# Kernel optimization log

Measured on AMD Instinct MI355X. Metric: run time of the kernel, lower is better.

Reference implementation:

```python
import jax, jax.numpy as jnp
import numpy as np

ALPHA = 0.2      # LeakyReLU negative slope
NEG_INF = -9e15  # mask value from the original code

def setup_inputs() -> dict:
    key = jax.random.key(0)
    k1, k2, k3, k4 = jax.random.split(key, 4)
    B, M, F_IN, F_OUT = 16, 2048, 128, 64
    h = jax.random.normal(k1, (B, M, F_IN), dtype=jnp.float32)
    adj = jax.random.randint(k2, (B, M, M), 0, 2, dtype=jnp.int32)
    W = jax.random.normal(k3, (F_IN, F_OUT), dtype=jnp.float32) * 0.1
    a = jax.random.normal(k4, (2 * F_OUT, 1), dtype=jnp.float32) * 0.1
    return {"h": h, "adj": adj, "W": W, "a": a}

def reference(h, adj, W, a):
    # h: [B,M,Fin], adj: [B,M,M], W: [Fin,E], a: [2E,1]
    Wh = jnp.matmul(h, W)                      # [B,M,E]
    E = Wh.shape[-1]
    a1, a2 = a[:E, 0], a[E:, 0]
    # decompose a^T [Wh_i || Wh_j] = (Wh_i . a1) + (Wh_j . a2)
    f1 = Wh @ a1                               # [B,M] (source/query term)
    f2 = Wh @ a2                               # [B,M] (target/key term)
    e = jax.nn.leaky_relu(f1[:, :, None] + f2[:, None, :], negative_slope=ALPHA)  # [B,M,M]
    scores = jnp.where(adj > 0, e, NEG_INF)
    attn = jax.nn.softmax(scores, axis=-1)     # [B,M,M]  (dropout p=0 / eval mode)
    h_prime = jnp.matmul(attn, Wh)             # [B,M,E]
    return jax.nn.elu(h_prime)                 # concat=True branch
```

## Files before the change

kernel.cpp:

```cpp
#include <hip/hip_runtime.h>


#define M_     2048
#define FIN_   128
#define F_     64
#define ALPHA_ 0.2f
#define HS_    132
#define WT_    132

typedef float  float4_ __attribute__((ext_vector_type(4)));
typedef short  short8  __attribute__((ext_vector_type(8)));
typedef int    int4_   __attribute__((ext_vector_type(4)));
typedef unsigned int u32x4 __attribute__((ext_vector_type(4)));
typedef unsigned short u16;
typedef unsigned int   u32;

static __device__ __forceinline__ u32 cvtpk(float lo, float hi) {
    u32 r;
    asm("v_cvt_pk_bf16_f32 %0, %1, %2" : "=v"(r) : "v"(lo), "v"(hi));
    return r;
}

static __device__ __forceinline__ int4_ ntload4(const int* p) {
    return __builtin_nontemporal_load((const int4_*)p);
}

__global__ __launch_bounds__(256, 4) void k_prep(
    const float* __restrict__ h, const float* __restrict__ W,
    const float* __restrict__ a, u16* __restrict__ hbf,
    float* __restrict__ f1all, float* __restrict__ f2all)
{
    __shared__ float a_s[2 * F_];
    __shared__ float wa1[FIN_], wa2[FIN_];
    __shared__ float hs[32 * HS_];

    const int tid = threadIdx.x;
    const u32 bid = blockIdx.x;
    const u32 lg  = (bid & 7) * 128 + (bid >> 3);
    const int b   = lg >> 6;
    const int t   = lg & 63;

    if (tid < 128) a_s[tid] = a[tid];

    const int tok = tid >> 3, f0 = (tid & 7) * 16;
    const float* hp = h + ((size_t)(b * M_ + t * 32 + tok)) * FIN_ + f0;
    float4_ x0 = *(const float4_*)hp;
    float4_ x1 = *(const float4_*)(hp + 4);
    float4_ x2 = *(const float4_*)(hp + 8);
    float4_ x3 = *(const float4_*)(hp + 12);
    __syncthreads();

    if (tid < FIN_) {
        float s1 = 0.f, s2 = 0.f;
#pragma unroll 8
        for (int n = 0; n < F_; ++n) {
            float wv = W[tid * F_ + n];
            s1 += wv * a_s[n];
            s2 += wv * a_s[F_ + n];
        }
        wa1[tid] = s1;
        wa2[tid] = s2;
    }

    float* hr = hs + tok * HS_ + f0;
    *(float4_*)(hr)      = x0;
    *(float4_*)(hr + 4)  = x1;
    *(float4_*)(hr + 8)  = x2;
    *(float4_*)(hr + 12) = x3;
    __syncthreads();

    {
        const int l = tid & 63, lc = l & 15, q = l >> 4;
        const int nt0 = (tid >> 6) * 2;
        u32x4* ob = (u32x4*)hbf + ((size_t)(b * 64 + t)) * 8 * 64;
#pragma unroll
        for (int ni = 0; ni < 2; ++ni) {
            const int nt = nt0 + ni;
            const float* cp = hs + (q * 8) * HS_ + nt * 16 + lc;
            u32x4 wv;
            wv[0] = cvtpk(cp[0 * HS_], cp[1 * HS_]);
            wv[1] = cvtpk(cp[2 * HS_], cp[3 * HS_]);
            wv[2] = cvtpk(cp[4 * HS_], cp[5 * HS_]);
            wv[3] = cvtpk(cp[6 * HS_], cp[7 * HS_]);
            ob[nt * 64 + l] = wv;
        }
    }

    {
        const int r = tid >> 3, k0 = (tid & 7) * 16;
        const float* rp = hs + r * HS_ + k0;
        float s1 = 0.f, s2 = 0.f;
#pragma unroll
        for (int k = 0; k < 16; ++k) {
            s1 += rp[k] * wa1[k0 + k];
            s2 += rp[k] * wa2[k0 + k];
        }
        s1 += __shfl_xor(s1, 1, 64); s2 += __shfl_xor(s2, 1, 64);
        s1 += __shfl_xor(s1, 2, 64); s2 += __shfl_xor(s2, 2, 64);
        s1 += __shfl_xor(s1, 4, 64); s2 += __shfl_xor(s2, 4, 64);
        if ((tid & 7) == 0) {
            f1all[b * M_ + t * 32 + r] = s1;
            f2all[b * M_ + t * 32 + r] = s2;
        }
    }
}

__global__ __launch_bounds__(256, 4) void k_main(
    const int* __restrict__ adj, const u16* __restrict__ hbf,
    const float* __restrict__ f1all, const float* __restrict__ f2all,
    const float* __restrict__ W, float* __restrict__ out)
{
    __shared__ char  dyn[WT_ * 32 * 4];
    __shared__ float dens2[64];

    float* f2s  = (float*)dyn;
    float* Tsum = (float*)dyn;

    const int tid  = threadIdx.x;
    const int w    = tid >> 6;
    const int l    = tid & 63;
    const int lc   = l & 15;
    const int quad = l >> 4;
    const int wr   = w & 1;
    const int wh   = w >> 1;

    const u32 bid = blockIdx.x;
    const u32 lg  = (bid & 7) * 128 + (bid >> 3);
    const int b   = lg >> 6;
    const int i0  = (lg & 63) * 32;
    const int rowbase = i0 + wr * 16;

    {
        const int o = tid * 8;
        float4_ v0 = *(const float4_*)(f2all + b * M_ + o);
        float4_ v1 = *(const float4_*)(f2all + b * M_ + o + 4);
        *(float4_*)(f2s + o)     = v0;
        *(float4_*)(f2s + o + 4) = v1;
    }

    const float f1r = f1all[b * M_ + rowbase + lc];
    const int* aprow = adj + ((size_t)(b * M_ + rowbase + lc)) * M_ + quad * 8;
    const u32x4* hb  = (const u32x4*)hbf + ((size_t)b * 64) * 8 * 64 + l;

    const int t0 = wh * 32;
    const int tE = t0 + 31;

    int4_ aA0 = ntload4(aprow + t0 * 32);
    int4_ aA1 = ntload4(aprow + t0 * 32 + 4);
    int4_ aB0 = ntload4(aprow + (t0 + 1) * 32);
    int4_ aB1 = ntload4(aprow + (t0 + 1) * 32 + 4);

    __syncthreads();

    float denacc = 0.f;
    float4_ acc[8];
#pragma unroll
    for (int nt = 0; nt < 8; ++nt) acc[nt] = (float4_){0.f, 0.f, 0.f, 0.f};

#define SC(GE, GO, AE, AO, IDX)                                 \
        {                                                       \
            float xe = f1r + (GE); xe = fmaxf(xe, ALPHA_ * xe); \
            float xo = f1r + (GO); xo = fmaxf(xo, ALPHA_ * xo); \
            float ee = ((AE) > 0) ? __expf(xe) : 0.f;           \
            float eo = ((AO) > 0) ? __expf(xo) : 0.f;           \
            u32 pk = cvtpk(ee, eo);                             \
            d += __uint_as_float(pk << 16);                     \
            d += __uint_as_float(pk & 0xFFFF0000u);             \
            pw[IDX] = pk;                                       \
        }

#define STAGE(T, A0, A1)                                                      \
    {                                                                         \
        const int tp = ((T) + 2 <= tE) ? (T) + 2 : tE;                        \
        u32x4 bb[8];                                                          \
        _Pragma("unroll")                                                     \
        for (int nt = 0; nt < 8; ++nt) bb[nt] = hb[((T) * 8 + nt) * 64];      \
        __builtin_amdgcn_sched_barrier(0);                                    \
        float4_ g0 = *(const float4_*)(f2s + (T) * 32 + quad * 8);            \
        float4_ g1 = *(const float4_*)(f2s + (T) * 32 + quad * 8 + 4);        \
        u32x4 pw;                                                             \
        float d = 0.f;                                                        \
        SC(g0[0], g0[1], A0[0], A0[1], 0)                                     \
        SC(g0[2], g0[3], A0[2], A0[3], 1)                                     \
        SC(g1[0], g1[1], A1[0], A1[1], 2)                                     \
        SC(g1[2], g1[3], A1[2], A1[3], 3)                                     \
        denacc += d;                                                          \
        const short8 af = __builtin_bit_cast(short8, pw);                     \
        A0 = ntload4(aprow + tp * 32);                                        \
        A1 = ntload4(aprow + tp * 32 + 4);                                    \
        __builtin_amdgcn_sched_barrier(0);                                    \
        _Pragma("unroll")                                                     \
        for (int nt = 0; nt < 8; ++nt)                                        \
            acc[nt] = __builtin_amdgcn_mfma_f32_16x16x32_bf16(                \
                af, __builtin_bit_cast(short8, bb[nt]), acc[nt], 0, 0, 0);    \
    }

    for (int o = 0; o < 16; ++o) {
        STAGE(t0 + 2 * o,     aA0, aA1)
        STAGE(t0 + 2 * o + 1, aB0, aB1)
    }
#undef STAGE
#undef SC

    denacc += __shfl_xor(denacc, 16, 64);
    denacc += __shfl_xor(denacc, 32, 64);
    if (quad == 0) dens2[wh * 32 + wr * 16 + lc] = denacc;
    __syncthreads();

    if (wh == 0) {
#pragma unroll
        for (int nt = 0; nt < 8; ++nt)
#pragma unroll
            for (int mm = 0; mm < 4; ++mm)
                Tsum[(wr * 16 + quad * 4 + mm) * WT_ + nt * 16 + lc] = acc[nt][mm];
    }
    __syncthreads();
    if (wh == 1) {
#pragma unroll
        for (int nt = 0; nt < 8; ++nt)
#pragma unroll
            for (int mm = 0; mm < 4; ++mm)
                Tsum[(wr * 16 + quad * 4 + mm) * WT_ + nt * 16 + lc] += acc[nt][mm];
    }
    __syncthreads();

    {
        const int r  = tid >> 3;
        const int n0 = (tid & 7) * 8;
        const float den  = dens2[r] + dens2[32 + r];
        const float rden = (den > 0.f) ? (1.f / den) : 0.f;
        float u[8];
#pragma unroll
        for (int nn = 0; nn < 8; ++nn) u[nn] = 0.f;
#pragma unroll 4
        for (int k = 0; k < FIN_; ++k) {
            const float tv = Tsum[r * WT_ + k];
            float4_ wv0 = *(const float4_*)(W + k * F_ + n0);
            float4_ wv1 = *(const float4_*)(W + k * F_ + n0 + 4);
            u[0] += tv * wv0[0]; u[1] += tv * wv0[1];
            u[2] += tv * wv0[2]; u[3] += tv * wv0[3];
            u[4] += tv * wv1[0]; u[5] += tv * wv1[1];
            u[6] += tv * wv1[2]; u[7] += tv * wv1[3];
        }
        float4_ o0, o1;
#pragma unroll
        for (int nn = 0; nn < 8; ++nn) {
            float hp = u[nn] * rden;
            float o  = hp > 0.f ? hp : expm1f(hp);
            if (nn < 4) o0[nn] = o; else o1[nn - 4] = o;
        }
        float* op = out + ((size_t)(b * M_ + i0 + r)) * F_ + n0;
        *(float4_*)op       = o0;
        *(float4_*)(op + 4) = o1;
    }
}

extern "C" void kernel_launch(void* const* d_in, const int* in_sizes, int n_in,
                              void* d_out, int out_size, void* d_ws, size_t ws_size,
                              hipStream_t stream)
{
    (void)out_size; (void)ws_size;
    const float* h  = (const float*)d_in[0];
    const int* adjp = (const int*)d_in[1];
    const float* Wp = (const float*)d_in[2];
    const float* ap = (const float*)d_in[3];
    for (int i = 0; i < n_in; ++i) {
        long s = in_sizes[i];
        if      (s == 4194304L)  h    = (const float*)d_in[i];
        else if (s == 67108864L) adjp = (const int*)d_in[i];
        else if (s == 8192L)     Wp   = (const float*)d_in[i];
        else if (s == 128L)      ap   = (const float*)d_in[i];
    }
    u16*   hbf   = (u16*)d_ws;
    float* f1all = (float*)((char*)d_ws + (8u << 20));
    float* f2all = f1all + 16 * M_;
    k_prep<<<1024, 256, 0, stream>>>(h, Wp, ap, hbf, f1all, f2all);
    k_main<<<1024, 256, 0, stream>>>(adjp, hbf, f1all, f2all, Wp, (float*)d_out);
}
```

Before: 435.6 us.

## Stage Wh tiles in double-buffered LDS and give each block 64 rows

Each block now handles 64 query rows, with four waves each owning 16 rows across all 64 key tiles, replacing the split-K over two wave halves. The bf16 Wh tile for each step is loaded once into a double-buffered LDS ring and shared by all four waves instead of every wave reading it from global memory. This removes the cross-wave partial-sum reduction and cuts global Wh traffic, at the cost of a block-wide barrier per tile, more LDS, lower occupancy (launch bounds 2) and half as many blocks.

```diff
diff --git a/kernel.cpp b/kernel.cpp
--- a/kernel.cpp
+++ b/kernel.cpp
@@ -105,15 +105,16 @@
     }
 }
 
-__global__ __launch_bounds__(256, 4) void k_main(
+__global__ __launch_bounds__(256, 2) void k_main(
     const int* __restrict__ adj, const u16* __restrict__ hbf,
     const float* __restrict__ f1all, const float* __restrict__ f2all,
     const float* __restrict__ W, float* __restrict__ out)
 {
-    __shared__ char  dyn[WT_ * 32 * 4];
-    __shared__ float dens2[64];
-
-    float* f2s  = (float*)dyn;
+    __shared__ char  dyn[64 * WT_ * 4];
+    __shared__ float dens[64];
+
+    u32x4* lbuf = (u32x4*)dyn;
+    float* f2s  = (float*)(dyn + 16384);
     float* Tsum = (float*)dyn;
 
     const int tid  = threadIdx.x;
@@ -121,14 +122,11 @@
     const int l    = tid & 63;
     const int lc   = l & 15;
     const int quad = l >> 4;
-    const int wr   = w & 1;
-    const int wh   = w >> 1;
 
     const u32 bid = blockIdx.x;
-    const u32 lg  = (bid & 7) * 128 + (bid >> 3);
-    const int b   = lg >> 6;
-    const int i0  = (lg & 63) * 32;
-    const int rowbase = i0 + wr * 16;
+    const u32 lg  = (bid & 7) * 64 + (bid >> 3);
+    const int b   = lg >> 5;
+    const int i0  = (lg & 31) * 64;
 
     {
         const int o = tid * 8;
@@ -138,17 +136,20 @@
         *(float4_*)(f2s + o + 4) = v1;
     }
 
-    const float f1r = f1all[b * M_ + rowbase + lc];
-    const int* aprow = adj + ((size_t)(b * M_ + rowbase + lc)) * M_ + quad * 8;
-    const u32x4* hb  = (const u32x4*)hbf + ((size_t)b * 64) * 8 * 64 + l;
-
-    const int t0 = wh * 32;
-    const int tE = t0 + 31;
-
-    int4_ aA0 = ntload4(aprow + t0 * 32);
-    int4_ aA1 = ntload4(aprow + t0 * 32 + 4);
-    int4_ aB0 = ntload4(aprow + (t0 + 1) * 32);
-    int4_ aB1 = ntload4(aprow + (t0 + 1) * 32 + 4);
+    const float f1r = f1all[b * M_ + i0 + w * 16 + lc];
+    const int* aprow = adj + ((size_t)(b * M_ + i0 + w * 16 + lc)) * M_ + quad * 8;
+    const u32x4* hbs = (const u32x4*)hbf + (size_t)b * 32768;
+
+    {
+        u32x4 s0 = hbs[tid];
+        u32x4 s1 = hbs[256 + tid];
+        lbuf[tid]       = s0;
+        lbuf[256 + tid] = s1;
+    }
+    int4_ aA0 = ntload4(aprow);
+    int4_ aA1 = ntload4(aprow + 4);
+    int4_ aB0 = ntload4(aprow + 32);
+    int4_ aB1 = ntload4(aprow + 36);
 
     __syncthreads();
 
@@ -171,11 +172,15 @@
 
 #define STAGE(T, A0, A1)                                                      \
     {                                                                         \
-        const int tp = ((T) + 2 <= tE) ? (T) + 2 : tE;                        \
+        const int ts = ((T) < 63) ? (T) + 1 : 63;                             \
+        const int tp = ((T) < 62) ? (T) + 2 : 63;                             \
+        u32x4 s0 = hbs[ts * 512 + tid];                                       \
+        u32x4 s1 = hbs[ts * 512 + 256 + tid];                                 \
+        __builtin_amdgcn_sched_barrier(0);                                    \
+        const u32x4* lc_ = lbuf + ((T) & 1) * 512;                            \
         u32x4 bb[8];                                                          \
         _Pragma("unroll")                                                     \
-        for (int nt = 0; nt < 8; ++nt) bb[nt] = hb[((T) * 8 + nt) * 64];      \
-        __builtin_amdgcn_sched_barrier(0);                                    \
+        for (int nt = 0; nt < 8; ++nt) bb[nt] = lc_[nt * 64 + l];             \
         float4_ g0 = *(const float4_*)(f2s + (T) * 32 + quad * 8);            \
         float4_ g1 = *(const float4_*)(f2s + (T) * 32 + quad * 8 + 4);        \
         u32x4 pw;                                                             \
@@ -188,46 +193,43 @@
         const short8 af = __builtin_bit_cast(short8, pw);                     \
         A0 = ntload4(aprow + tp * 32);                                        \
         A1 = ntload4(aprow + tp * 32 + 4);                                    \
-        __builtin_amdgcn_sched_barrier(0);                                    \
         _Pragma("unroll")                                                     \
         for (int nt = 0; nt < 8; ++nt)                                        \
             acc[nt] = __builtin_amdgcn_mfma_f32_16x16x32_bf16(                \
                 af, __builtin_bit_cast(short8, bb[nt]), acc[nt], 0, 0, 0);    \
-    }
-
-    for (int o = 0; o < 16; ++o) {
-        STAGE(t0 + 2 * o,     aA0, aA1)
-        STAGE(t0 + 2 * o + 1, aB0, aB1)
+        __builtin_amdgcn_sched_barrier(0);                                    \
+        u32x4* ln_ = lbuf + (((T) + 1) & 1) * 512;                            \
+        ln_[tid]       = s0;                                                  \
+        ln_[256 + tid] = s1;                                                  \
+        asm volatile("s_waitcnt lgkmcnt(0)" ::: "memory");                    \
+        __builtin_amdgcn_s_barrier();                                         \
+        __builtin_amdgcn_sched_barrier(0);                                    \
+    }
+
+    for (int o2 = 0; o2 < 32; ++o2) {
+        STAGE(2 * o2,     aA0, aA1)
+        STAGE(2 * o2 + 1, aB0, aB1)
     }
 #undef STAGE
 #undef SC
 
     denacc += __shfl_xor(denacc, 16, 64);
     denacc += __shfl_xor(denacc, 32, 64);
-    if (quad == 0) dens2[wh * 32 + wr * 16 + lc] = denacc;
-    __syncthreads();
-
-    if (wh == 0) {
-#pragma unroll
-        for (int nt = 0; nt < 8; ++nt)
-#pragma unroll
-            for (int mm = 0; mm < 4; ++mm)
-                Tsum[(wr * 16 + quad * 4 + mm) * WT_ + nt * 16 + lc] = acc[nt][mm];
-    }
-    __syncthreads();
-    if (wh == 1) {
-#pragma unroll
-        for (int nt = 0; nt < 8; ++nt)
-#pragma unroll
-            for (int mm = 0; mm < 4; ++mm)
-                Tsum[(wr * 16 + quad * 4 + mm) * WT_ + nt * 16 + lc] += acc[nt][mm];
-    }
-    __syncthreads();
-
-    {
-        const int r  = tid >> 3;
+    if (quad == 0) dens[w * 16 + lc] = denacc;
+    __syncthreads();
+
+#pragma unroll
+    for (int nt = 0; nt < 8; ++nt)
+#pragma unroll
+        for (int mm = 0; mm < 4; ++mm)
+            Tsum[(w * 16 + quad * 4 + mm) * WT_ + nt * 16 + lc] = acc[nt][mm];
+    __syncthreads();
+
+#pragma unroll
+    for (int rr = 0; rr < 2; ++rr) {
+        const int r  = (tid >> 3) + rr * 32;
         const int n0 = (tid & 7) * 8;
-        const float den  = dens2[r] + dens2[32 + r];
+        const float den  = dens[r];
         const float rden = (den > 0.f) ? (1.f / den) : 0.f;
         float u[8];
 #pragma unroll
@@ -275,5 +277,5 @@
     float* f1all = (float*)((char*)d_ws + (8u << 20));
     float* f2all = f1all + 16 * M_;
     k_prep<<<1024, 256, 0, stream>>>(h, Wp, ap, hbf, f1all, f2all);
-    k_main<<<1024, 256, 0, stream>>>(adjp, hbf, f1all, f2all, Wp, (float*)d_out);
-}
+    k_main<<<512, 256, 0, stream>>>(adjp, hbf, f1all, f2all, Wp, (float*)d_out);
+}
```

Measured after the change: 416.7 us. 4.3% less time.
